# Kernel tuning notes

Hardware: AMD Instinct MI355X
Metric: run time of the kernel (lower is better)

The kernel has to match this reference:

```python
import jax, jax.numpy as jnp
import numpy as np

N_HEAD = 12

def setup_inputs() -> dict:
    key = jax.random.key(0)
    ks = jax.random.split(key, 5)
    B, T, C = 2, 2048, 768
    s = 1.0 / np.sqrt(C)
    return {
        "x": jax.random.normal(ks[0], (B, T, C), dtype=jnp.float32),
        "W_qkv": jax.random.normal(ks[1], (C, 3 * C), dtype=jnp.float32) * s,
        "b_qkv": jnp.zeros((3 * C,), dtype=jnp.float32),
        "W_proj": jax.random.normal(ks[2], (C, C), dtype=jnp.float32) * s,
        "b_proj": jnp.zeros((C,), dtype=jnp.float32),
    }

def reference(x, W_qkv, b_qkv, W_proj, b_proj):
    B, T, C = x.shape
    H = N_HEAD
    D = C // H
    qkv = x @ W_qkv + b_qkv                      # [B,T,3C]
    qkv = qkv.reshape(B, T, 3, H, D)
    q = jnp.transpose(qkv[:, :, 0], (0, 2, 1, 3))  # [B,H,T,D]
    k = jnp.transpose(qkv[:, :, 1], (0, 2, 1, 3))
    v = jnp.transpose(qkv[:, :, 2], (0, 2, 1, 3))
    scale = 1.0 / np.sqrt(D).astype(np.float32)
    att = jnp.einsum('bhqd,bhkd->bhqk', q, k) * scale  # [B,H,T,T]
    causal = jnp.tril(jnp.ones((T, T), dtype=bool))
    att = jnp.where(causal, att, -jnp.inf)
    att = jax.nn.softmax(att, axis=-1)
    out = jnp.einsum('bhqk,bhkd->bhqd', att, v)   # [B,H,T,D]
    out = jnp.transpose(out, (0, 2, 1, 3)).reshape(B, T, C)
    return out @ W_proj + b_proj
```

## Files before the change

### kernel.cpp

```cpp
#include <hip/hip_runtime.h>
#include <stdint.h>

typedef short short8 __attribute__((ext_vector_type(8)));
typedef short short4v __attribute__((ext_vector_type(4)));
typedef float f32x4 __attribute__((ext_vector_type(4)));
typedef unsigned int u32x2 __attribute__((ext_vector_type(2)));
typedef unsigned int u32x4 __attribute__((ext_vector_type(4)));
typedef unsigned short u16;
typedef unsigned int u32;

#define T_ 2048
#define QK_SCALE 0.180336878f

__device__ inline u16 f2bf(float f) {
  unsigned u = __builtin_bit_cast(unsigned, f);
  u += 0x7fffu + ((u >> 16) & 1u);
  return (u16)(u >> 16);
}

__device__ inline u32 cvt_pk_bf16(float lo, float hi) {
  u32 r;
  asm("v_cvt_pk_bf16_f32 %0, %1, %2" : "=v"(r) : "v"(lo), "v"(hi));
  return r;
}

__device__ inline f32x4 mfma_bf16(short8 a, short8 b, f32x4 c) {
  return __builtin_amdgcn_mfma_f32_16x16x32_bf16(a, b, c, 0, 0, 0);
}

__device__ inline void gload16(const u16* g, u16* l) {
  __builtin_amdgcn_global_load_lds(
      (const __attribute__((address_space(1))) void*)g,
      (__attribute__((address_space(3))) void*)l, 16, 0, 0);
}


__device__ inline void tile_transpose(const float* __restrict__ W, u16* __restrict__ Wt,
                                      int R, int Ccols, int c0, int r0, int t,
                                      float (*tile)[33]) {
  int tr = t >> 3, tc = (t & 7) * 4;
  float4 v = *(const float4*)&W[(size_t)(r0 + tr) * Ccols + c0 + tc];
  tile[tr][tc + 0] = v.x; tile[tr][tc + 1] = v.y;
  tile[tr][tc + 2] = v.z; tile[tr][tc + 3] = v.w;
  __syncthreads();
  short4v o;
#pragma unroll
  for (int i = 0; i < 4; ++i) o[i] = (short)f2bf(tile[tc + i][tr]);
  *(short4v*)&Wt[(size_t)(c0 + tr) * R + r0 + tc] = o;
}

__global__ __launch_bounds__(256) void prep_kernel(const float* __restrict__ x,
                                                   const float* __restrict__ Wqkv,
                                                   const float* __restrict__ Wproj,
                                                   u16* __restrict__ xb,
                                                   u16* __restrict__ wqkvT,
                                                   u16* __restrict__ wprojT) {
  __shared__ float tile[32][33];
  int bid = blockIdx.x, t = threadIdx.x;
  if (bid < 3072) {
    int i = (bid * 256 + t) * 4;
    float4 v = *(const float4*)&x[i];
    short4v o;
    o[0] = (short)f2bf(v.x); o[1] = (short)f2bf(v.y);
    o[2] = (short)f2bf(v.z); o[3] = (short)f2bf(v.w);
    *(short4v*)&xb[i] = o;
  } else if (bid < 3072 + 1728) {
    int t2 = bid - 3072;
    tile_transpose(Wqkv, wqkvT, 768, 2304, (t2 % 72) * 32, (t2 / 72) * 32, t, tile);
  } else {
    int t3 = bid - 4800;
    tile_transpose(Wproj, wprojT, 768, 768, (t3 % 24) * 32, (t3 / 24) * 32, t, tile);
  }
}


template <int MODE, int MTILE>
__global__ __launch_bounds__(256) void gemm_kernel(const u16* __restrict__ A,
                                                   const u16* __restrict__ Bt,
                                                   const float* __restrict__ bias,
                                                   u16* __restrict__ qb,
                                                   u16* __restrict__ kb,
                                                   u16* __restrict__ vpb,
                                                   float* __restrict__ out) {
  constexpr int MF = MTILE / 32;
  __shared__ u16 S[MTILE * 64 + 8192];
  u16* As = S;
  u16* Bs = S + MTILE * 64;
  int tid = threadIdx.x, w = tid >> 6, l = tid & 63, lg = l >> 4, lr = l & 15;
  int nwg = gridDim.x * gridDim.y;
  int hw = blockIdx.y * gridDim.x + blockIdx.x;
  int logical = (hw & 7) * (nwg >> 3) + (hw >> 3);
  int n0 = (logical % gridDim.x) * 128, m0 = (logical / gridDim.x) * MTILE;
  int wm = (w >> 1) * (MTILE / 2), wn = (w & 1) * 64;
  f32x4 acc[MF][4] = {};
  int rsub = l >> 3;
  int sc = ((l & 7) ^ rsub) * 8;
  for (int kt = 0; kt < 12; ++kt) {
    int k0 = kt * 64;
    __syncthreads();
#pragma unroll
    for (int j = 0; j < MF; ++j) {
      int row = w * (MTILE / 4) + j * 8 + rsub;
      gload16(&A[(size_t)(m0 + row) * 768 + k0 + sc], &As[(w * MF + j) * 512]);
    }
#pragma unroll
    for (int j = 0; j < 4; ++j) {
      int row = w * 32 + j * 8 + rsub;
      gload16(&Bt[(size_t)(n0 + row) * 768 + k0 + sc], &Bs[(w * 4 + j) * 512]);
    }
    __syncthreads();
    short8 a[MF][2], b[4][2];
#pragma unroll
    for (int h = 0; h < 2; ++h) {
#pragma unroll
      for (int mf = 0; mf < MF; ++mf) {
        int cw = ((h * 4 + lg) ^ (lr & 7)) * 8;
        a[mf][h] = *(const short8*)&As[(wm + mf * 16 + lr) * 64 + cw];
      }
#pragma unroll
      for (int nf = 0; nf < 4; ++nf) {
        int cw = ((h * 4 + lg) ^ (lr & 7)) * 8;
        b[nf][h] = *(const short8*)&Bs[(wn + nf * 16 + lr) * 64 + cw];
      }
    }
#pragma unroll
    for (int h = 0; h < 2; ++h)
#pragma unroll
      for (int mf = 0; mf < MF; ++mf)
#pragma unroll
        for (int nf = 0; nf < 4; ++nf)
          acc[mf][nf] = mfma_bf16(a[mf][h], b[nf][h], acc[mf][nf]);
  }

  if constexpr (MODE == 0) {
    int sec = (n0 >= 1536) ? 2 : (n0 >= 768 ? 1 : 0);
    int ncol0 = n0 - sec * 768;
    if (sec < 2) {
#pragma unroll
      for (int nf = 0; nf < 4; ++nf) {
        int nn = wn + nf * 16 + lr;
        float bv = bias[n0 + nn];
        int c = ncol0 + nn;
        int hh = c >> 6, d = c & 63;
#pragma unroll
        for (int mf = 0; mf < MF; ++mf)
#pragma unroll
          for (int rr = 0; rr < 4; ++rr) {
            int m = m0 + wm + mf * 16 + 4 * lg + rr;
            int bb = m >> 11, tt = m & 2047;
            int bh = bb * 12 + hh;
            float v = acc[mf][nf][rr] + bv;
            if (sec == 0) qb[((size_t)bh * T_ + tt) * 64 + d] = f2bf(v * QK_SCALE);
            else          kb[((size_t)bh * T_ + tt) * 64 + d] = f2bf(v);
          }
      }
    } else {
      __syncthreads();
#pragma unroll
      for (int nf = 0; nf < 4; ++nf) {
        int row = wn + nf * 16 + lr;
        float bv = bias[n0 + row];
        int swz = (row & 7) << 3;
#pragma unroll
        for (int mf = 0; mf < MF; ++mf) {
          int pcol0 = wm + (mf >> 1) * 32 + 8 * lg + 4 * (mf & 1);
          u32x2 pk;
          pk[0] = cvt_pk_bf16(acc[mf][nf][0] + bv, acc[mf][nf][1] + bv);
          pk[1] = cvt_pk_bf16(acc[mf][nf][2] + bv, acc[mf][nf][3] + bv);
          *(u32x2*)&S[row * MTILE + (pcol0 ^ swz)] = pk;
        }
      }
      __syncthreads();
      constexpr int CPT = MTILE / 2;
      int rowo = tid >> 1, half = tid & 1;
      int c = ncol0 + rowo;
      int d = c & 63, hh = c >> 6;
      int bh = (m0 >> 11) * 12 + hh;
      u16* dst = vpb + ((size_t)bh * 64 + d) * T_ + (m0 & 2047) + half * CPT;
      int swzo = (rowo & 7) << 3;
#pragma unroll
      for (int i = 0; i < CPT / 8; ++i) {
        int col = half * CPT + i * 8;
        uint4 v = *(const uint4*)&S[rowo * MTILE + (col ^ swzo)];
        *(uint4*)&dst[i * 8] = v;
      }
    }
  } else {
#pragma unroll
    for (int nf = 0; nf < 4; ++nf) {
      int n = n0 + wn + nf * 16 + lr;
      float bv = bias[n];
#pragma unroll
      for (int mf = 0; mf < MF; ++mf)
#pragma unroll
        for (int rr = 0; rr < 4; ++rr) {
          int m = m0 + wm + mf * 16 + 4 * lg + rr;
          out[(size_t)m * 768 + n] = acc[mf][nf][rr] + bv;
        }
    }
  }
}


__global__ __launch_bounds__(512) void attn_kernel(const u16* __restrict__ Q,
                                                   const u16* __restrict__ K,
                                                   const u16* __restrict__ Vp,
                                                   u16* __restrict__ O) {
  __shared__ u16 sh[32768];
  int tid = threadIdx.x;
  int w = tid >> 6, l = tid & 63, lg = l >> 4, lr = l & 15;
  int i = w >> 1, j = w & 1;
  int idx = blockIdx.x;
  int head = idx % 24;
  int qblk = 31 - idx / 24;
  int b = head / 12, h = head % 12;
  int q0 = qblk * 64;
  int q0w = q0 + i * 16;
  const u16* Qb = Q + (size_t)head * T_ * 64;
  const u16* Kb = K + (size_t)head * T_ * 64;
  const u16* Vb = Vp + (size_t)head * 64 * T_;

  short8 qf0 = *(const short8*)&Qb[(size_t)(q0w + lr) * 64 + 8 * lg];
  short8 qf1 = *(const short8*)&Qb[(size_t)(q0w + lr) * 64 + 32 + 8 * lg];

  f32x4 ao[4] = {};
  float lrow = 0.f;
  int rsub = l >> 3;
  int scs = ((l & 7) ^ rsub) * 8;
  int row = w * 8 + rsub;
  const int nt = qblk + 1;

  gload16(&Kb[(size_t)row * 64 + scs], &sh[w * 512]);
  gload16(&Vb[(size_t)row * T_ + scs], &sh[16384 + w * 512]);
  if (nt > 1) {
    gload16(&Kb[(size_t)(64 + row) * 64 + scs], &sh[4096 + w * 512]);
    gload16(&Vb[(size_t)row * T_ + 64 + scs], &sh[16384 + 4096 + w * 512]);
  }
  __syncthreads();

  for (int tp = 0; tp < nt; tp += 2) {
    int p = (tp >> 1) & 1;
    if (tp + 2 < nt) {
      int base = ((p ^ 1) * 2) * 4096;
      gload16(&Kb[(size_t)((tp + 2) * 64 + row) * 64 + scs], &sh[base + w * 512]);
      gload16(&Vb[(size_t)row * T_ + (tp + 2) * 64 + scs], &sh[16384 + base + w * 512]);
    }
    if (tp + 3 < nt) {
      int base = ((p ^ 1) * 2 + 1) * 4096;
      gload16(&Kb[(size_t)((tp + 3) * 64 + row) * 64 + scs], &sh[base + w * 512]);
      gload16(&Vb[(size_t)row * T_ + (tp + 3) * 64 + scs], &sh[16384 + base + w * 512]);
    }
#pragma unroll
    for (int sub = 0; sub < 2; ++sub) {
      int t = tp + sub;
      if (t < nt) {
        int k0 = t * 64;
        if (k0 + 32 * j <= q0w + 15) {
          const u16* ks = sh + (p * 2 + sub) * 4096;
          const u16* vs = sh + 16384 + (p * 2 + sub) * 4096;
          short8 ka0[2], ka1[2], va[4];
#pragma unroll
          for (int g = 0; g < 2; ++g) {
            int kg = 2 * j + g;
            ka0[g] = *(const short8*)&ks[(kg * 16 + lr) * 64 + ((lg ^ (lr & 7)) * 8)];
            ka1[g] = *(const short8*)&ks[(kg * 16 + lr) * 64 + (((4 + lg) ^ (lr & 7)) * 8)];
          }
#pragma unroll
          for (int dt = 0; dt < 4; ++dt)
            va[dt] = *(const short8*)&vs[(dt * 16 + lr) * 64 + (((4 * j + lg) ^ (lr & 7)) * 8)];
          f32x4 sm[2];
          __builtin_amdgcn_s_setprio(1);
#pragma unroll
          for (int g = 0; g < 2; ++g) {
            f32x4 z = {};
            z = mfma_bf16(ka0[g], qf0, z);
            z = mfma_bf16(ka1[g], qf1, z);
            sm[g] = z;
          }
          __builtin_amdgcn_s_setprio(0);
          float sv[8];
          float ps = 0.f;
          bool needmask = (t == nt - 1) && (32 * j + 31 > 16 * i);
          if (needmask) {
            int qa = q0w + lr;
#pragma unroll
            for (int g = 0; g < 2; ++g)
#pragma unroll
              for (int rr = 0; rr < 4; ++rr) {
                int key = k0 + (2 * j + g) * 16 + 4 * lg + rr;
                float x = (key <= qa) ? sm[g][rr] : -1e30f;
                float pv = __builtin_amdgcn_exp2f(x);
                sv[g * 4 + rr] = pv;
                ps += pv;
              }
          } else {
#pragma unroll
            for (int g = 0; g < 2; ++g)
#pragma unroll
              for (int rr = 0; rr < 4; ++rr) {
                float pv = __builtin_amdgcn_exp2f(sm[g][rr]);
                sv[g * 4 + rr] = pv;
                ps += pv;
              }
          }
          lrow += ps;
          u32x4 uu;
          uu[0] = cvt_pk_bf16(sv[0], sv[1]);
          uu[1] = cvt_pk_bf16(sv[2], sv[3]);
          uu[2] = cvt_pk_bf16(sv[4], sv[5]);
          uu[3] = cvt_pk_bf16(sv[6], sv[7]);
          short8 pb = __builtin_bit_cast(short8, uu);
          __builtin_amdgcn_s_setprio(1);
#pragma unroll
          for (int dt = 0; dt < 4; ++dt)
            ao[dt] = mfma_bf16(va[dt], pb, ao[dt]);
          __builtin_amdgcn_s_setprio(0);
        }
      }
    }
    __syncthreads();
  }

  lrow += __shfl_xor(lrow, 16);
  lrow += __shfl_xor(lrow, 32);

  float* aoL = (float*)sh;
  float* lrL = (float*)(sh + 8192);
  if (j == 1) {
#pragma unroll
    for (int dt = 0; dt < 4; ++dt)
      *(f32x4*)&aoL[(i * 64 + l) * 16 + dt * 4] = ao[dt];
    lrL[i * 64 + l] = lrow;
  }
  __syncthreads();
  if (j == 0) {
#pragma unroll
    for (int dt = 0; dt < 4; ++dt)
      ao[dt] += *(const f32x4*)&aoL[(i * 64 + l) * 16 + dt * 4];
    lrow += lrL[i * 64 + l];
    u16* ow = sh + 9216 + i * 1152;
    float inv = 1.0f / lrow;
#pragma unroll
    for (int dt = 0; dt < 4; ++dt) {
      u32x2 pk;
      pk[0] = cvt_pk_bf16(ao[dt][0] * inv, ao[dt][1] * inv);
      pk[1] = cvt_pk_bf16(ao[dt][2] * inv, ao[dt][3] * inv);
      *(u32x2*)&ow[lr * 72 + dt * 16 + 4 * lg] = pk;
    }
    asm volatile("s_waitcnt lgkmcnt(0)" ::: "memory");
    int r = l >> 2, hc = l & 3;
    const u16* srow = sh + 9216 + i * 1152 + r * 72 + hc * 16;
    u16* dst = O + ((size_t)(b * T_ + q0w + r)) * 768 + h * 64 + hc * 16;
    *(uint4*)&dst[0] = *(const uint4*)&srow[0];
    *(uint4*)&dst[8] = *(const uint4*)&srow[8];
  }
}


extern "C" void kernel_launch(void* const* d_in, const int* in_sizes, int n_in,
                              void* d_out, int out_size, void* d_ws, size_t ws_size,
                              hipStream_t stream) {
  const float* x     = (const float*)d_in[0];
  const float* Wqkv  = (const float*)d_in[1];
  const float* bqkv  = (const float*)d_in[2];
  const float* Wproj = (const float*)d_in[3];
  const float* bproj = (const float*)d_in[4];
  float* out = (float*)d_out;
  char* ws = (char*)d_ws;
  u16* xb     = (u16*)(ws);
  u16* wqkvT  = (u16*)(ws + 6291456);
  u16* wprojT = (u16*)(ws + 9830400);
  u16* qb     = (u16*)(ws + 11010048);
  u16* kb     = (u16*)(ws + 17301504);
  u16* vpb    = (u16*)(ws + 23592960);
  u16* ob     = (u16*)(ws + 29884416);

  prep_kernel<<<5376, 256, 0, stream>>>(x, Wqkv, Wproj, xb, wqkvT, wprojT);
  gemm_kernel<0, 64><<<dim3(18, 64), 256, 0, stream>>>(xb, wqkvT, bqkv, qb, kb, vpb, nullptr);
  attn_kernel<<<768, 512, 0, stream>>>(qb, kb, vpb, ob);
  gemm_kernel<1, 32><<<dim3(6, 128), 256, 0, stream>>>(ob, wprojT, bproj, nullptr, nullptr, nullptr, out);
}
```

Baseline: 73.96 us.

## Double-buffer GEMM shared-memory tiles to prefetch next K-slice during MFMA

The GEMM main loop now keeps two LDS buffers for the A and B tiles. The first K-slice is loaded before the loop, and each iteration issues the global-to-LDS loads for the next slice before running the MFMAs on the current one. This cuts the loop to one barrier per iteration instead of two and hides global load latency behind compute. In exchange the kernel uses twice as much shared memory, which may reduce the number of resident workgroups per CU.

```diff
diff --git a/kernel.cpp b/kernel.cpp
--- a/kernel.cpp
+++ b/kernel.cpp
@@ -83,9 +83,10 @@
                                                    u16* __restrict__ vpb,
                                                    float* __restrict__ out) {
   constexpr int MF = MTILE / 32;
-  __shared__ u16 S[MTILE * 64 + 8192];
+  constexpr int ABUF = MTILE * 64;
+  __shared__ u16 S[2 * ABUF + 2 * 8192];
   u16* As = S;
-  u16* Bs = S + MTILE * 64;
+  u16* Bs = S + 2 * ABUF;
   int tid = threadIdx.x, w = tid >> 6, l = tid & 63, lg = l >> 4, lr = l & 15;
   int nwg = gridDim.x * gridDim.y;
   int hw = blockIdx.y * gridDim.x + blockIdx.x;
@@ -95,32 +96,48 @@
   f32x4 acc[MF][4] = {};
   int rsub = l >> 3;
   int sc = ((l & 7) ^ rsub) * 8;
+
+#pragma unroll
+  for (int j = 0; j < MF; ++j) {
+    int row = w * (MTILE / 4) + j * 8 + rsub;
+    gload16(&A[(size_t)(m0 + row) * 768 + sc], &As[(w * MF + j) * 512]);
+  }
+#pragma unroll
+  for (int j = 0; j < 4; ++j) {
+    int row = w * 32 + j * 8 + rsub;
+    gload16(&Bt[(size_t)(n0 + row) * 768 + sc], &Bs[(w * 4 + j) * 512]);
+  }
+  __syncthreads();
+
   for (int kt = 0; kt < 12; ++kt) {
-    int k0 = kt * 64;
-    __syncthreads();
-#pragma unroll
-    for (int j = 0; j < MF; ++j) {
-      int row = w * (MTILE / 4) + j * 8 + rsub;
-      gload16(&A[(size_t)(m0 + row) * 768 + k0 + sc], &As[(w * MF + j) * 512]);
-    }
-#pragma unroll
-    for (int j = 0; j < 4; ++j) {
-      int row = w * 32 + j * 8 + rsub;
-      gload16(&Bt[(size_t)(n0 + row) * 768 + k0 + sc], &Bs[(w * 4 + j) * 512]);
-    }
-    __syncthreads();
+    int p = kt & 1;
+    if (kt + 1 < 12) {
+      int k1 = (kt + 1) * 64;
+#pragma unroll
+      for (int j = 0; j < MF; ++j) {
+        int row = w * (MTILE / 4) + j * 8 + rsub;
+        gload16(&A[(size_t)(m0 + row) * 768 + k1 + sc], &As[(p ^ 1) * ABUF + (w * MF + j) * 512]);
+      }
+#pragma unroll
+      for (int j = 0; j < 4; ++j) {
+        int row = w * 32 + j * 8 + rsub;
+        gload16(&Bt[(size_t)(n0 + row) * 768 + k1 + sc], &Bs[(p ^ 1) * 8192 + (w * 4 + j) * 512]);
+      }
+    }
+    const u16* Ap = As + p * ABUF;
+    const u16* Bp = Bs + p * 8192;
     short8 a[MF][2], b[4][2];
 #pragma unroll
     for (int h = 0; h < 2; ++h) {
 #pragma unroll
       for (int mf = 0; mf < MF; ++mf) {
         int cw = ((h * 4 + lg) ^ (lr & 7)) * 8;
-        a[mf][h] = *(const short8*)&As[(wm + mf * 16 + lr) * 64 + cw];
+        a[mf][h] = *(const short8*)&Ap[(wm + mf * 16 + lr) * 64 + cw];
       }
 #pragma unroll
       for (int nf = 0; nf < 4; ++nf) {
         int cw = ((h * 4 + lg) ^ (lr & 7)) * 8;
-        b[nf][h] = *(const short8*)&Bs[(wn + nf * 16 + lr) * 64 + cw];
+        b[nf][h] = *(const short8*)&Bp[(wn + nf * 16 + lr) * 64 + cw];
       }
     }
 #pragma unroll
@@ -130,6 +147,7 @@
 #pragma unroll
         for (int nf = 0; nf < 4; ++nf)
           acc[mf][nf] = mfma_bf16(a[mf][h], b[nf][h], acc[mf][nf]);
+    __syncthreads();
   }
 
   if constexpr (MODE == 0) {
@@ -155,7 +173,6 @@
           }
       }
     } else {
-      __syncthreads();
 #pragma unroll
       for (int nf = 0; nf < 4; ++nf) {
         int row = wn + nf * 16 + lr;
```

After: 71.92 us, median of 2. 1.03x faster.
